# Optimization experiments

Measured on AMD Instinct MI355X. Metric: run time of the kernel, lower is better.

Reference implementation:

```python
import jax, jax.numpy as jnp
import numpy as np
import math

TOP_K = 2
CAPACITY_FACTOR = 1.25


def setup_inputs() -> dict:
    key = jax.random.key(0)
    ks = jax.random.split(key, 5)
    T, H, F, E = 16384, 1024, 4096, 8
    s = lambda d: 1.0 / np.sqrt(d)
    return {
        "tokens": jax.random.normal(ks[0], (T, H), jnp.float32),
        "w_router": jax.random.normal(ks[1], (H, E), jnp.float32) * s(H),
        "w_gate": jax.random.normal(ks[2], (E, H, F), jnp.float32) * s(H),
        "w_up": jax.random.normal(ks[3], (E, H, F), jnp.float32) * s(H),
        "w_down": jax.random.normal(ks[4], (E, F, H), jnp.float32) * s(F),
    }


def _moe_forward(tokens, w_router, w_gate, w_up, w_down):
    T, H = tokens.shape
    E = w_gate.shape[0]
    C = int(math.ceil(CAPACITY_FACTOR * T / E))  # per-expert capacity, static

    # --- Router: softmax over experts, top-k, renormalized weights ---
    logits = tokens @ w_router                       # (T, E)
    probs = jax.nn.softmax(logits, axis=-1)
    topv, topi = jax.lax.top_k(probs, TOP_K)         # (T, K)
    weights = topv / jnp.sum(topv, axis=-1, keepdims=True)

    # --- Dispatch ranks replicating torch loop order: k-slot major, token index minor ---
    onehot = jax.nn.one_hot(topi, E, dtype=jnp.int32)            # (T, K, E)
    counts = onehot.sum(axis=0)                                  # (K, E) tokens per (slot, expert)
    slot_off = jnp.concatenate(
        [jnp.zeros((1, E), jnp.int32), jnp.cumsum(counts, axis=0)[:-1]], axis=0
    )                                                            # (K, E) exclusive offset over k
    rank = jnp.cumsum(onehot, axis=0) - 1 + slot_off[None]       # (T, K, E)
    rank_tk = jnp.take_along_axis(rank, topi[..., None], axis=-1).squeeze(-1)  # (T, K)

    keep = rank_tk < C                                           # tokens beyond capacity are dropped
    slot = jnp.where(keep, rank_tk, C)                           # dropped -> trash slot C

    e_flat = topi.reshape(-1)                                    # (T*K,)
    s_flat = slot.reshape(-1)
    tok_rep = jnp.broadcast_to(tokens[:, None, :], (T, TOP_K, H)).reshape(-1, H)

    # Gather tokens into per-expert capacity buffers (extra trash row at slot C)
    buf = jnp.zeros((E, C + 1, H), tokens.dtype).at[e_flat, s_flat].set(tok_rep)
    x = buf[:, :C]                                               # (E, C, H)

    # --- SwiGLU expert FFN, batched over experts (grouped GEMM) ---
    h = jax.nn.silu(jnp.einsum('ech,ehf->ecf', x, w_gate)) * jnp.einsum('ech,ehf->ecf', x, w_up)
    y = jnp.einsum('ecf,efh->ech', h, w_down)                    # (E, C, H)

    # --- Weighted scatter back to token positions ---
    out_flat = y[e_flat, jnp.minimum(s_flat, C - 1)]             # (T*K, H)
    w_eff = (weights * keep.astype(weights.dtype)).reshape(-1, 1)
    return (out_flat * w_eff).reshape(T, TOP_K, H).sum(axis=1)   # (T, H)


def reference(tokens, w_router, w_gate, w_up, w_down):
    return _moe_forward(tokens, w_router, w_gate, w_up, w_down)
```

## Files before the change

### kernel.cpp

```cpp
#include <hip/hip_runtime.h>
#include <hip/hip_bf16.h>
#include <stdint.h>

#define T_TOK 16384
#define HDIM  1024
#define FDIM  4096
#define NE    8
#define CAP   2560

typedef __attribute__((ext_vector_type(8))) __bf16 bf16x8;
typedef __attribute__((ext_vector_type(4))) float  f32x4;

#define MFMA_BF16 __builtin_amdgcn_mfma_f32_16x16x32_bf16
#define VMCNT2()  asm volatile("s_waitcnt vmcnt(2)" ::: "memory")
#define VMCNT3()  asm volatile("s_waitcnt vmcnt(3)" ::: "memory")
#define VMCNT4()  asm volatile("s_waitcnt vmcnt(4)" ::: "memory")
#define LGKM0()   asm volatile("s_waitcnt lgkmcnt(0)" ::: "memory")
#define BAR()     __builtin_amdgcn_s_barrier()
#define SCHED0()  __builtin_amdgcn_sched_barrier(0)

__device__ __forceinline__ unsigned short f2bf(float f) {
  union { float f; unsigned u; } c; c.f = f;
  unsigned u = c.u;
  return (unsigned short)((u + 0x7FFFu + ((u >> 16) & 1u)) >> 16);
}

__device__ __forceinline__ void gload_lds16(const void* g, void* lds) {
  __builtin_amdgcn_global_load_lds((const __attribute__((address_space(1))) void*)g,
                                   (__attribute__((address_space(3))) void*)lds,
                                   16, 0, 0);
}

__global__ __launch_bounds__(256)
void transpose_cvt(const float* __restrict__ in, unsigned short* __restrict__ out,
                   int R, int Cc) {
  __shared__ unsigned short tile[64][68];
  int e  = blockIdx.z;
  int rb = blockIdx.y << 6, cb = blockIdx.x << 6;
  const float* inp = in + (size_t)e * R * Cc;
  unsigned short* op = out + (size_t)e * R * Cc;
  int lc  = threadIdx.x & 63;
  int lr0 = threadIdx.x >> 6;
#pragma unroll
  for (int rr = 0; rr < 64; rr += 4) {
    int r = rr + lr0;
    float v = inp[(size_t)(rb + r) * Cc + cb + lc];
    tile[lc][r] = f2bf(v);
  }
  __syncthreads();
  int c0 = threadIdx.x >> 3;
  int h0 = (threadIdx.x & 7) << 3;
#pragma unroll
  for (int cc = 0; cc < 64; cc += 32) {
    int c = cc + c0;
    uint2 v0 = *(const uint2*)&tile[c][h0];
    uint2 v1 = *(const uint2*)&tile[c][h0 + 4];
    uint4 v; v.x = v0.x; v.y = v0.y; v.z = v1.x; v.w = v1.y;
    *(uint4*)(op + (size_t)(cb + c) * R + rb + h0) = v;
  }
}

__global__ __launch_bounds__(256)
void transpose_cvt_gu(const float* __restrict__ in, unsigned short* __restrict__ out, int up) {
  __shared__ unsigned short tile[64][68];
  int e  = blockIdx.z;
  int rb = blockIdx.y << 6, cb = blockIdx.x << 6;
  const float* inp = in + (size_t)e * HDIM * FDIM;
  unsigned short* op = out + (size_t)e * 2 * FDIM * HDIM;
  int lc  = threadIdx.x & 63;
  int lr0 = threadIdx.x >> 6;
#pragma unroll
  for (int rr = 0; rr < 64; rr += 4) {
    int r = rr + lr0;
    float v = inp[(size_t)(rb + r) * FDIM + cb + lc];
    tile[lc][r] = f2bf(v);
  }
  __syncthreads();
  int c0 = threadIdx.x >> 3;
  int h0 = (threadIdx.x & 7) << 3;
#pragma unroll
  for (int cc = 0; cc < 64; cc += 32) {
    int c = cc + c0;
    int C = cb + c;
    int orow = ((C >> 5) << 6) + (C & 31) + (up << 5);
    uint2 v0 = *(const uint2*)&tile[c][h0];
    uint2 v1 = *(const uint2*)&tile[c][h0 + 4];
    uint4 v; v.x = v0.x; v.y = v0.y; v.z = v1.x; v.w = v1.y;
    *(uint4*)(op + (size_t)orow * HDIM + rb + h0) = v;
  }
}

__global__ __launch_bounds__(256)
void router_kernel(const float* __restrict__ tokens, const float* __restrict__ wr,
                   int* __restrict__ topsel, float* __restrict__ wts) {
  int lane = threadIdx.x & 63;
  int t = (blockIdx.x << 2) + (threadIdx.x >> 6);
  const float* tok = tokens + (size_t)t * HDIM;
  float acc[8];
#pragma unroll
  for (int i = 0; i < 8; ++i) acc[i] = 0.f;
#pragma unroll
  for (int j = 0; j < 4; ++j) {
    int h0 = j * 256 + lane * 4;
    float4 tv = *(const float4*)(tok + h0);
    const float* w = wr + (size_t)h0 * 8;
#pragma unroll
    for (int q = 0; q < 4; ++q) {
      float xv = ((const float*)&tv)[q];
      float4 wa = *(const float4*)(w + q * 8);
      float4 wb = *(const float4*)(w + q * 8 + 4);
      acc[0] += xv * wa.x; acc[1] += xv * wa.y; acc[2] += xv * wa.z; acc[3] += xv * wa.w;
      acc[4] += xv * wb.x; acc[5] += xv * wb.y; acc[6] += xv * wb.z; acc[7] += xv * wb.w;
    }
  }
#pragma unroll
  for (int off = 1; off < 64; off <<= 1) {
#pragma unroll
    for (int i = 0; i < 8; ++i) acc[i] += __shfl_xor(acc[i], off, 64);
  }
  if (lane == 0) {
    int e0 = 0; float v0 = acc[0];
#pragma unroll
    for (int i = 1; i < 8; ++i) if (acc[i] > v0) { v0 = acc[i]; e0 = i; }
    int e1 = -1; float v1 = -3.4e38f;
#pragma unroll
    for (int i = 0; i < 8; ++i) if (i != e0 && acc[i] > v1) { v1 = acc[i]; e1 = i; }
    float w0 = 1.f / (1.f + __expf(v1 - v0));
    topsel[t * 2] = e0; topsel[t * 2 + 1] = e1;
    wts[t * 2] = w0;    wts[t * 2 + 1] = 1.f - w0;
  }
}

__global__ __launch_bounds__(256)
void dispatch_kernel(const int* __restrict__ topsel, int* __restrict__ slot,
                     int* __restrict__ src_tok) {
  int e = blockIdx.x;
  int w = threadIdx.x >> 6, lane = threadIdx.x & 63;
  __shared__ int gcnt[2][256];
  __shared__ int tot[2];
#pragma unroll
  for (int k = 0; k < 2; ++k)
    for (int g = w; g < 256; g += 4) {
      int ch = topsel[(g * 64 + lane) * 2 + k];
      unsigned long long m = __ballot(ch == e);
      if (lane == 0) gcnt[k][g] = __popcll(m);
    }
  __syncthreads();
  if (w < 2) {
    int k = w;
    int c0 = gcnt[k][lane * 4], c1 = gcnt[k][lane * 4 + 1];
    int c2 = gcnt[k][lane * 4 + 2], c3 = gcnt[k][lane * 4 + 3];
    int s = c0 + c1 + c2 + c3;
    int inc = s;
#pragma unroll
    for (int off = 1; off < 64; off <<= 1) {
      int v = __shfl_up(inc, off, 64);
      if (lane >= off) inc += v;
    }
    int base = inc - s;
    gcnt[k][lane * 4] = base;
    gcnt[k][lane * 4 + 1] = base + c0;
    gcnt[k][lane * 4 + 2] = base + c0 + c1;
    gcnt[k][lane * 4 + 3] = base + c0 + c1 + c2;
    if (lane == 63) tot[k] = inc;
  }
  __syncthreads();
#pragma unroll
  for (int k = 0; k < 2; ++k) {
    int kbase = (k == 1) ? tot[0] : 0;
    for (int g = w; g < 256; g += 4) {
      int t = g * 64 + lane;
      int ch = topsel[t * 2 + k];
      unsigned long long m = __ballot(ch == e);
      if (ch == e) {
        unsigned long long lmask = lane ? (~0ull >> (64 - lane)) : 0ull;
        int r = kbase + gcnt[k][g] + __popcll(m & lmask);
        if (r < CAP) { slot[t * 2 + k] = r; src_tok[e * CAP + r] = t; }
        else         { slot[t * 2 + k] = -1; }
      }
    }
  }
}

__global__ __launch_bounds__(128)
void gather_x(const float* __restrict__ tokens, const int* __restrict__ src_tok,
              unsigned short* __restrict__ x) {
  int s = blockIdx.x;
  int t = src_tok[s];
  unsigned short* xr = x + (size_t)s * HDIM + threadIdx.x * 8;
  uint4 v = {0u, 0u, 0u, 0u};
  if (t >= 0) {
    const float* tr = tokens + (size_t)t * HDIM + threadIdx.x * 8;
    float4 a = *(const float4*)tr;
    float4 b = *(const float4*)(tr + 4);
    v.x = (unsigned)f2bf(a.x) | ((unsigned)f2bf(a.y) << 16);
    v.y = (unsigned)f2bf(a.z) | ((unsigned)f2bf(a.w) << 16);
    v.z = (unsigned)f2bf(b.x) | ((unsigned)f2bf(b.y) << 16);
    v.w = (unsigned)f2bf(b.z) | ((unsigned)f2bf(b.w) << 16);
  }
  *(uint4*)xr = v;
}

template<int BN>
__device__ __forceinline__ void mainloop8(const unsigned short* __restrict__ Ag,
                                          const unsigned short* __restrict__ Bg,
                                          int lda, int ldb, int nkt,
                                          unsigned short* lds, f32x4 (&acc)[4][BN / 32]) {
  constexpr int NF   = BN / 64;
  constexpr int AELB = 256 * 64 * 2;
  constexpr int BELB = BN * 64 * 2;
  constexpr int BHB  = (BN / 2) * 128;
  int tid = threadIdx.x, lane = tid & 63, wid = tid >> 6;
  int qr = wid >> 1, qc = wid & 1;
  int fr = lane & 15, fg = lane >> 4;

  char* ldsc = (char*)lds;
  int swz0 = ((fg       ^ (fr & 7)) << 4);
  int swz1 = (((4 | fg) ^ (fr & 7)) << 4);
  const char* a_b0 = ldsc + (qr * 32 + fr) * 128 + swz0;
  const char* a_b1 = ldsc + (qr * 32 + fr) * 128 + swz1;
  const char* b_b0 = ldsc + 2 * AELB + (qc * (NF * 16) + fr) * 128 + swz0;
  const char* b_b1 = ldsc + 2 * AELB + (qc * (NF * 16) + fr) * 128 + swz1;

  int srow = tid >> 3;
  int sl8  = ((tid & 7) ^ (srow & 7)) * 8;

  auto stA = [&](int mh, int kt, int pb) {
    char* dst = ldsc + pb + mh * 16384;
    gload_lds16(Ag + (size_t)(mh * 128 + srow) * lda + kt + sl8, dst + tid * 16);
    gload_lds16(Ag + (size_t)(mh * 128 + 64 + srow) * lda + kt + sl8, dst + tid * 16 + 8192);
  };
  auto stB = [&](int nh, int kt, int qb) {
    char* dst = ldsc + 2 * AELB + qb + nh * BHB;
    gload_lds16(Bg + (size_t)(nh * (BN / 2) + srow) * ldb + kt + sl8, dst + tid * 16);
    if constexpr (BN == 256)
      gload_lds16(Bg + (size_t)(nh * (BN / 2) + 64 + srow) * ldb + kt + sl8,
                  dst + tid * 16 + 8192);
  };

  bf16x8 aA[2][2], aB[2][2], bA[NF][2], bB[NF][2];
  auto rdA = [&](bf16x8 (&dst)[2][2], int mh, int pb) {
#pragma unroll
    for (int mf = 0; mf < 2; ++mf) {
      dst[mf][0] = *(const bf16x8*)(a_b0 + pb + mh * 16384 + mf * 2048);
      dst[mf][1] = *(const bf16x8*)(a_b1 + pb + mh * 16384 + mf * 2048);
    }
  };
  auto rdB = [&](bf16x8 (&dst)[NF][2], int nh, int qb) {
#pragma unroll
    for (int nf = 0; nf < NF; ++nf) {
      dst[nf][0] = *(const bf16x8*)(b_b0 + qb + nh * BHB + nf * 2048);
      dst[nf][1] = *(const bf16x8*)(b_b1 + qb + nh * BHB + nf * 2048);
    }
  };
  auto mmq = [&](bf16x8 (&A)[2][2], bf16x8 (&B)[NF][2], int mh, int nh) {
    __builtin_amdgcn_s_setprio(1);
#pragma unroll
    for (int mf = 0; mf < 2; ++mf)
#pragma unroll
      for (int nf = 0; nf < NF; ++nf)
#pragma unroll
        for (int kk = 0; kk < 2; ++kk)
          acc[mh * 2 + mf][nh * NF + nf] =
              MFMA_BF16(A[mf][kk], B[nf][kk], acc[mh * 2 + mf][nh * NF + nf], 0, 0, 0);
    __builtin_amdgcn_s_setprio(0);
  };

  int ktp = (nkt > 1 ? 64 : 0);
  stA(0, 0, 0); stB(1, 0, 0); stB(0, 0, 0); stA(1, 0, 0);
  stA(0, ktp, AELB); stB(1, ktp, BELB);
  if constexpr (BN == 256) VMCNT4(); else VMCNT3();
  BAR();
  rdA(aA, 0, 0); rdB(bA, 0, 0);

  for (int t = 0; t < nkt; ++t) {
    int p0 = (t & 1) ? AELB : 0, p1 = AELB - p0;
    int q0 = (t & 1) ? BELB : 0, q1 = BELB - q0;
    int kt1 = ((t + 1 < nkt) ? t + 1 : nkt - 1) * 64;
    int kt2 = ((t + 2 < nkt) ? t + 2 : nkt - 1) * 64;

    LGKM0(); SCHED0();
    rdA(aB, 1, p0);
    stB(0, kt1, q1);
    mmq(aA, bA, 0, 0);
    BAR();

    LGKM0(); SCHED0();
    rdB(bB, 1, q0);
    stA(1, kt1, p1);
    mmq(aB, bA, 1, 0);
    VMCNT2();
    BAR();

    LGKM0(); SCHED0();
    rdB(bA, 0, q1);
    stA(0, kt2, p0);
    mmq(aB, bB, 1, 1);
    BAR();

    LGKM0(); SCHED0();
    stB(1, kt2, q0);
    mmq(aA, bB, 0, 1);
    SCHED0();
    rdA(aA, 0, p1);
    if constexpr (BN == 256) VMCNT4(); else VMCNT3();
    BAR();
  }
}

__global__ __launch_bounds__(512, 1)
void gemm1_kernel(const unsigned short* __restrict__ x, const unsigned short* __restrict__ wgu,
                  unsigned short* __restrict__ h) {
  __shared__ unsigned short lds[2 * 256 * 64 + 2 * 256 * 64];
  int flat = blockIdx.x;
  int e = flat & 7, idx = flat >> 3;
  int c = idx >> 4, i = idx & 15;
  int cbx = c / 5, cby = c % 5;
  int bx = cbx * 8 + (i & 7), by = cby * 2 + (i >> 3);
  const unsigned short* Ag = x   + ((size_t)e * CAP + (size_t)by * 256) * HDIM;
  const unsigned short* Bg = wgu + ((size_t)e * 2 * FDIM + (size_t)bx * 256) * HDIM;
  f32x4 acc[4][8];
#pragma unroll
  for (int m = 0; m < 4; ++m)
#pragma unroll
    for (int n = 0; n < 8; ++n) acc[m][n] = (f32x4){0.f, 0.f, 0.f, 0.f};
  mainloop8<256>(Ag, Bg, HDIM, HDIM, HDIM / 64, lds, acc);

  int lane = threadIdx.x & 63, wid = threadIdx.x >> 6;
  int qr = wid >> 1, qc = wid & 1, fr = lane & 15, fg = lane >> 4;
  size_t rbase = (size_t)e * CAP + by * 256;
#pragma unroll
  for (int mi = 0; mi < 4; ++mi) {
    int row0 = (mi >> 1) * 128 + qr * 32 + (mi & 1) * 16 + fg * 4;
#pragma unroll
    for (int nh = 0; nh < 2; ++nh)
#pragma unroll
      for (int nf = 0; nf < 2; ++nf) {
        int fcol = bx * 128 + (nh * 2 + qc) * 32 + nf * 16 + fr;
#pragma unroll
        for (int v = 0; v < 4; ++v) {
          float g = acc[mi][nh * 4 + nf][v];
          float u = acc[mi][nh * 4 + nf + 2][v];
          float s = g / (1.f + __expf(-g));
          h[(rbase + row0 + v) * FDIM + fcol] = f2bf(s * u);
        }
      }
  }
}

__global__ __launch_bounds__(512, 1)
void gemm2_kernel(const unsigned short* __restrict__ h, const unsigned short* __restrict__ wdT,
                  float* __restrict__ y) {
  __shared__ unsigned short lds[2 * 256 * 64 + 2 * 128 * 64];
  int flat = blockIdx.x;
  int e = flat & 7, idx = flat >> 3;
  int c = idx >> 4, i = idx & 15;
  int bx = i & 7, by = c * 2 + (i >> 3);
  const unsigned short* Ag = h   + ((size_t)e * CAP  + (size_t)by * 256) * FDIM;
  const unsigned short* Bg = wdT + ((size_t)e * HDIM + (size_t)bx * 128) * FDIM;
  f32x4 acc[4][4];
#pragma unroll
  for (int m = 0; m < 4; ++m)
#pragma unroll
    for (int n = 0; n < 4; ++n) acc[m][n] = (f32x4){0.f, 0.f, 0.f, 0.f};
  mainloop8<128>(Ag, Bg, FDIM, FDIM, FDIM / 64, lds, acc);

  int lane = threadIdx.x & 63, wid = threadIdx.x >> 6;
  int qr = wid >> 1, qc = wid & 1, fr = lane & 15, fg = lane >> 4;
  size_t rbase = (size_t)e * CAP + by * 256;
#pragma unroll
  for (int mi = 0; mi < 4; ++mi) {
    int row0 = (mi >> 1) * 128 + qr * 32 + (mi & 1) * 16 + fg * 4;
#pragma unroll
    for (int ni = 0; ni < 4; ++ni) {
      int col = bx * 128 + (ni >> 1) * 64 + qc * 32 + (ni & 1) * 16 + fr;
#pragma unroll
      for (int v = 0; v < 4; ++v)
        y[(rbase + row0 + v) * HDIM + col] = acc[mi][ni][v];
    }
  }
}

__global__ __launch_bounds__(256)
void combine_kernel(const float* __restrict__ y, const int* __restrict__ topsel,
                    const int* __restrict__ slot, const float* __restrict__ wts,
                    float* __restrict__ out) {
  int t = blockIdx.x;
  int i = threadIdx.x * 4;
  float4 s = {0.f, 0.f, 0.f, 0.f};
#pragma unroll
  for (int k = 0; k < 2; ++k) {
    int sl = slot[t * 2 + k];
    if (sl >= 0) {
      int e = topsel[t * 2 + k];
      float w = wts[t * 2 + k];
      float4 v = *(const float4*)(y + ((size_t)e * CAP + sl) * HDIM + i);
      s.x += w * v.x; s.y += w * v.y; s.z += w * v.z; s.w += w * v.w;
    }
  }
  *(float4*)(out + (size_t)t * HDIM + i) = s;
}

extern "C" void kernel_launch(void* const* d_in, const int* in_sizes, int n_in,
                              void* d_out, int out_size, void* d_ws, size_t ws_size,
                              hipStream_t stream) {
  const float* tokens   = (const float*)d_in[0];
  const float* w_router = (const float*)d_in[1];
  const float* w_gate   = (const float*)d_in[2];
  const float* w_up     = (const float*)d_in[3];
  const float* w_down   = (const float*)d_in[4];
  float* out = (float*)d_out;
  char* ws = (char*)d_ws;

  const size_t WGU = (size_t)NE * 2 * FDIM * HDIM * 2;
  const size_t WD  = (size_t)NE * HDIM * FDIM * 2;
  const size_t XB  = (size_t)NE * CAP * HDIM * 2;
  const size_t HB  = (size_t)NE * CAP * FDIM * 2;
  unsigned short* wguT = (unsigned short*)(ws);
  unsigned short* wdT  = (unsigned short*)(ws + WGU);
  unsigned short* xbuf = (unsigned short*)(ws + WGU + WD);
  unsigned short* hbuf = (unsigned short*)(ws + WGU + WD + XB);
  float* ybuf = (float*)(ws);
  char* tail = ws + WGU + WD + XB + HB;
  int*   topsel  = (int*)tail;
  float* wtsv    = (float*)(tail + (size_t)T_TOK * 2 * 4);
  int*   slotv   = (int*)(tail + (size_t)T_TOK * 2 * 8);
  int*   src_tok = (int*)(tail + (size_t)T_TOK * 2 * 12);

  hipMemsetAsync(src_tok, 0xFF, (size_t)NE * CAP * 4, stream);

  transpose_cvt_gu<<<dim3(FDIM / 64, HDIM / 64, NE), 256, 0, stream>>>(w_gate, wguT, 0);
  transpose_cvt_gu<<<dim3(FDIM / 64, HDIM / 64, NE), 256, 0, stream>>>(w_up,   wguT, 1);
  transpose_cvt<<<dim3(HDIM / 64, FDIM / 64, NE), 256, 0, stream>>>(w_down, wdT, FDIM, HDIM);

  router_kernel<<<T_TOK / 4, 256, 0, stream>>>(tokens, w_router, topsel, wtsv);
  dispatch_kernel<<<NE, 256, 0, stream>>>(topsel, slotv, src_tok);
  gather_x<<<NE * CAP, 128, 0, stream>>>(tokens, src_tok, xbuf);

  gemm1_kernel<<<2560, 512, 0, stream>>>(xbuf, wguT, hbuf);
  gemm2_kernel<<<640, 512, 0, stream>>>(hbuf, wdT, ybuf);

  combine_kernel<<<T_TOK, 256, 0, stream>>>(ybuf, topsel, slotv, wtsv, out);
}
```

Baseline: 808.1 us.

## Restructure GEMM main loop to single-tile prefetch with phased barriers

Changes the GEMM k-loop pipeline from a two-tile-ahead prefetch, where LDS reads overlap the MFMAs of the previous phase, to a one-tile-ahead scheme. Each phase now issues LDS reads and global-to-LDS stores, hits a barrier, waits on lgkmcnt, then runs its MFMAs under a separate barrier. The likely aim is to cut LDS hazards or register pressure and simplify synchronization. In exchange there are twice as many barriers per iteration and less overlap between LDS reads and compute, which could stall the matrix cores.

```diff
diff --git a/kernel.cpp b/kernel.cpp
--- a/kernel.cpp
+++ b/kernel.cpp
@@ -12,10 +12,10 @@
 typedef __attribute__((ext_vector_type(4))) float  f32x4;
 
 #define MFMA_BF16 __builtin_amdgcn_mfma_f32_16x16x32_bf16
-#define VMCNT2()  asm volatile("s_waitcnt vmcnt(2)" ::: "memory")
 #define VMCNT3()  asm volatile("s_waitcnt vmcnt(3)" ::: "memory")
 #define VMCNT4()  asm volatile("s_waitcnt vmcnt(4)" ::: "memory")
 #define LGKM0()   asm volatile("s_waitcnt lgkmcnt(0)" ::: "memory")
+#define LGKM8()   asm volatile("s_waitcnt lgkmcnt(8)" ::: "memory")
 #define BAR()     __builtin_amdgcn_s_barrier()
 #define SCHED0()  __builtin_amdgcn_sched_barrier(0)
 
@@ -266,45 +266,45 @@
     __builtin_amdgcn_s_setprio(0);
   };
 
-  int ktp = (nkt > 1 ? 64 : 0);
-  stA(0, 0, 0); stB(1, 0, 0); stB(0, 0, 0); stA(1, 0, 0);
-  stA(0, ktp, AELB); stB(1, ktp, BELB);
+  stA(0, 0, 0); stB(0, 0, 0); stA(1, 0, 0); stB(1, 0, 0);
   if constexpr (BN == 256) VMCNT4(); else VMCNT3();
   BAR();
-  rdA(aA, 0, 0); rdB(bA, 0, 0);
 
   for (int t = 0; t < nkt; ++t) {
     int p0 = (t & 1) ? AELB : 0, p1 = AELB - p0;
     int q0 = (t & 1) ? BELB : 0, q1 = BELB - q0;
     int kt1 = ((t + 1 < nkt) ? t + 1 : nkt - 1) * 64;
-    int kt2 = ((t + 2 < nkt) ? t + 2 : nkt - 1) * 64;
-
+
+    rdA(aA, 0, p0);
+    rdB(bA, 0, q0);
+    stA(0, kt1, p1);
+    if constexpr (BN == 256) LGKM8();
+    SCHED0(); BAR();
     LGKM0(); SCHED0();
+    mmq(aA, bA, 0, 0);
+    if constexpr (BN == 256) VMCNT4(); else VMCNT3();
+    SCHED0(); BAR();
+
     rdA(aB, 1, p0);
     stB(0, kt1, q1);
-    mmq(aA, bA, 0, 0);
-    BAR();
-
+    SCHED0(); BAR();
     LGKM0(); SCHED0();
+    mmq(aB, bA, 1, 0);
+    if constexpr (BN == 256) VMCNT4(); else VMCNT3();
+    SCHED0(); BAR();
+
     rdB(bB, 1, q0);
     stA(1, kt1, p1);
-    mmq(aB, bA, 1, 0);
-    VMCNT2();
-    BAR();
-
+    SCHED0(); BAR();
     LGKM0(); SCHED0();
-    rdB(bA, 0, q1);
-    stA(0, kt2, p0);
     mmq(aB, bB, 1, 1);
-    BAR();
-
-    LGKM0(); SCHED0();
-    stB(1, kt2, q0);
+    SCHED0(); BAR();
+
+    stB(1, kt1, q1);
+    SCHED0(); BAR();
     mmq(aA, bB, 0, 1);
-    SCHED0();
-    rdA(aA, 0, p1);
     if constexpr (BN == 256) VMCNT4(); else VMCNT3();
-    BAR();
+    SCHED0(); BAR();
   }
 }
 
```

After: 804.0 us. Within noise of the previous version (-0.5%).
